# Kernel tuning notes

Measured on AMD Instinct MI355X. Metric: run time of the kernel, lower is better.

## Reference

```python
import jax, jax.numpy as jnp
import numpy as np

D = 512       # d_model
H = 8         # n_heads
L = 6         # n_blocks
DFF = 2048    # d_ffn
IN_DIM = 4096
OUT_DIM = 1000
B = 8
S = 512
DK = D // H
EPS = 1e-5
NEG = -1e9    # masked_fill value from source (-1000000000.0)

# sinusoidal positional encoding table (matches Positional_Encoding)
_pos = np.arange(5000)[:, None].astype(np.float64)
_div = np.exp(np.arange(0, D, 2) * (-np.log(10000.0) / D))
_pe = np.zeros((5000, D), np.float32)
_pe[:, 0::2] = np.sin(_pos * _div)
_pe[:, 1::2] = np.cos(_pos * _div)
PE = jnp.asarray(_pe)


def _ln(x, g, b):
    m = jnp.mean(x, -1, keepdims=True)
    v = jnp.var(x, -1, keepdims=True)
    return (x - m) * jax.lax.rsqrt(v + EPS) * g + b


def _attn(q, k, v, causal):
    # q:[B,Sq,D], k/v:[B,Sk,D] -> multi-head attention with source's quirky mask
    b, sq, _ = q.shape
    sk = k.shape[1]
    q = q.reshape(b, sq, H, DK).transpose(0, 2, 1, 3)
    k = k.reshape(b, sk, H, DK).transpose(0, 2, 1, 3)
    v = v.reshape(b, sk, H, DK).transpose(0, 2, 1, 3)
    s = jnp.einsum('bhqd,bhkd->bhqk', q, k) / jnp.sqrt(jnp.asarray(DK, q.dtype))
    mask = s != 0.0  # faithful: source masks positions where score == padding (0)
    if causal:
        mask = mask & jnp.tril(jnp.ones((sq, sk), bool))
    s = jnp.where(mask, s, NEG)
    p = jax.nn.softmax(s, axis=-1)
    o = jnp.einsum('bhqk,bhkd->bhqd', p, v)
    return o.transpose(0, 2, 1, 3).reshape(b, sq, D)


def _ffn(x, w1, b1, w2, b2):
    return jax.nn.relu(x @ w1 + b1) @ w2 + b2


def setup_inputs() -> dict:
    key = jax.random.key(0)
    ks = iter(jax.random.split(key, 40))

    def w(shape, s=0.02):
        return jax.random.normal(next(ks), shape, jnp.float32) * s

    inp = {}
    inp['x'] = jax.random.randint(next(ks), (B, S), 0, IN_DIM)
    inp['target'] = jax.random.randint(next(ks), (B,), 0, OUT_DIM)
    inp['in_emb'] = w((IN_DIM, D), 1.0)
    inp['out_emb'] = w((OUT_DIM, D), 1.0)
    # encoder params (stacked over layers)
    inp['enc_qkv_w'] = w((L, 3, D, D))
    inp['enc_qkv_b'] = w((L, 3, D))
    inp['enc_ln1_g'] = jnp.ones((L, D), jnp.float32)
    inp['enc_ln1_b'] = jnp.zeros((L, D), jnp.float32)
    inp['enc_ffn1_w'] = w((L, D, DFF))
    inp['enc_ffn1_b'] = w((L, DFF))
    inp['enc_ffn2_w'] = w((L, DFF, D))
    inp['enc_ffn2_b'] = w((L, D))
    inp['enc_ln2_g'] = jnp.ones((L, D), jnp.float32)
    inp['enc_ln2_b'] = jnp.zeros((L, D), jnp.float32)
    # decoder params
    inp['dec_qkv1_w'] = w((L, 3, D, D))
    inp['dec_qkv1_b'] = w((L, 3, D))
    inp['dec_ln1_g'] = jnp.ones((L, D), jnp.float32)
    inp['dec_ln1_b'] = jnp.zeros((L, D), jnp.float32)
    inp['dec_qkv2_w'] = w((L, 3, D, D))
    inp['dec_qkv2_b'] = w((L, 3, D))
    inp['dec_ln2_g'] = jnp.ones((L, D), jnp.float32)
    inp['dec_ln2_b'] = jnp.zeros((L, D), jnp.float32)
    inp['dec_ffn1_w'] = w((L, D, DFF))
    inp['dec_ffn1_b'] = w((L, DFF))
    inp['dec_ffn2_w'] = w((L, DFF, D))
    inp['dec_ffn2_b'] = w((L, D))
    inp['dec_ln3_g'] = jnp.ones((L, D), jnp.float32)
    inp['dec_ln3_b'] = jnp.zeros((L, D), jnp.float32)
    inp['out_w'] = w((D, OUT_DIM))
    inp['out_b'] = w((OUT_DIM,))
    return inp


def reference(x, target, in_emb, out_emb,
              enc_qkv_w, enc_qkv_b, enc_ln1_g, enc_ln1_b,
              enc_ffn1_w, enc_ffn1_b, enc_ffn2_w, enc_ffn2_b,
              enc_ln2_g, enc_ln2_b,
              dec_qkv1_w, dec_qkv1_b, dec_ln1_g, dec_ln1_b,
              dec_qkv2_w, dec_qkv2_b, dec_ln2_g, dec_ln2_b,
              dec_ffn1_w, dec_ffn1_b, dec_ffn2_w, dec_ffn2_b,
              dec_ln3_g, dec_ln3_b, out_w, out_b):
    scale = jnp.sqrt(jnp.float32(D))
    # encoder: embed tokens + positional encoding (dropout is identity at eval)
    e = in_emb[x] * scale + PE[None, :S]
    for i in range(L):
        q = e @ enc_qkv_w[i, 0] + enc_qkv_b[i, 0]
        k = e @ enc_qkv_w[i, 1] + enc_qkv_b[i, 1]
        v = e @ enc_qkv_w[i, 2] + enc_qkv_b[i, 2]
        e = _ln(_attn(q, k, v, False) + e, enc_ln1_g[i], enc_ln1_b[i])
        e = _ln(e + _ffn(e, enc_ffn1_w[i], enc_ffn1_b[i], enc_ffn2_w[i], enc_ffn2_b[i]),
                enc_ln2_g[i], enc_ln2_b[i])
    # decoder: target.unsqueeze(1) -> seq len 1
    d = out_emb[target][:, None, :] * scale + PE[None, :1]
    for i in range(L):
        q = d @ dec_qkv1_w[i, 0] + dec_qkv1_b[i, 0]
        k = d @ dec_qkv1_w[i, 1] + dec_qkv1_b[i, 1]
        v = d @ dec_qkv1_w[i, 2] + dec_qkv1_b[i, 2]
        d = _ln(_attn(q, k, v, True) + d, dec_ln1_g[i], dec_ln1_b[i])
        q = d @ dec_qkv2_w[i, 0] + dec_qkv2_b[i, 0]
        k = e @ dec_qkv2_w[i, 1] + dec_qkv2_b[i, 1]
        v = e @ dec_qkv2_w[i, 2] + dec_qkv2_b[i, 2]
        d = _ln(_attn(q, k, v, False) + d, dec_ln2_g[i], dec_ln2_b[i])
        d = _ln(d + _ffn(d, dec_ffn1_w[i], dec_ffn1_b[i], dec_ffn2_w[i], dec_ffn2_b[i]),
                dec_ln3_g[i], dec_ln3_b[i])
    return d @ out_w + out_b  # [B, 1, OUT_DIM] logits (source never applies its softmax)
```

## Files before the change

kernel.cpp:

```cpp
#include <hip/hip_runtime.h>
#include <hip/hip_bf16.h>

#define DM 512
#define NH 8
#define DK 64
#define SEQ 512
#define NB 8
#define NL 6
#define DFF 2048
#define OUTD 1000
#define EMB_SCALE 22.627416997969522f
#define PE_C (-0.017988946039015984)

typedef __bf16 bf16x8 __attribute__((ext_vector_type(8)));
typedef __bf16 bf16x4 __attribute__((ext_vector_type(4)));
typedef float f32x4 __attribute__((ext_vector_type(4)));

__device__ __forceinline__ void load16_lds(const __bf16* g, __bf16* l) {
  __builtin_amdgcn_global_load_lds(
      (const __attribute__((address_space(1))) void*)g,
      (__attribute__((address_space(3))) void*)l, 16, 0, 0);
}

__global__ __launch_bounds__(256) void pe_kernel(float* __restrict__ pe) {
  int s = blockIdx.x;
  int d2 = threadIdx.x;
  double div = exp((double)(2 * d2) * PE_C);
  double arg = (double)s * div;
  pe[(size_t)s * DM + 2 * d2] = (float)sin(arg);
  pe[(size_t)s * DM + 2 * d2 + 1] = (float)cos(arg);
}

__global__ __launch_bounds__(256) void embed_enc(const int* __restrict__ x,
                                                 const float* __restrict__ emb,
                                                 const float* __restrict__ pe,
                                                 float* __restrict__ e,
                                                 __bf16* __restrict__ eb) {
  int idx = blockIdx.x * 256 + threadIdx.x;
  int d = idx & (DM - 1);
  int bs = idx >> 9;
  int s = bs & (SEQ - 1);
  int tok = x[bs];
  float v = emb[(size_t)tok * DM + d] * EMB_SCALE + pe[(size_t)s * DM + d];
  e[idx] = v;
  eb[idx] = (__bf16)v;
}

__global__ __launch_bounds__(256) void embed_dec(const int* __restrict__ t,
                                                 const float* __restrict__ emb,
                                                 float* __restrict__ dd) {
  int idx = blockIdx.x * 256 + threadIdx.x;
  int d = idx & (DM - 1);
  int b = idx >> 9;
  float pe = (d & 1) ? 1.0f : 0.0f;
  dd[idx] = emb[(size_t)t[b] * DM + d] * EMB_SCALE + pe;
}

__global__ __launch_bounds__(256) void transpose_w(const float* __restrict__ W,
                                                   __bf16* __restrict__ WT,
                                                   int K, int N) {
  __shared__ float t[32][33];
  size_t off = (size_t)blockIdx.z * K * N;
  W += off; WT += off;
  int k0 = blockIdx.y * 32, n0 = blockIdx.x * 32;
  int tx = threadIdx.x & 7, ty = threadIdx.x >> 3;
  float4 v = *(const float4*)&W[(size_t)(k0 + ty) * N + n0 + tx * 4];
  t[ty][tx * 4 + 0] = v.x; t[ty][tx * 4 + 1] = v.y;
  t[ty][tx * 4 + 2] = v.z; t[ty][tx * 4 + 3] = v.w;
  __syncthreads();
  bf16x4 o;
  o[0] = (__bf16)t[tx * 4 + 0][ty];
  o[1] = (__bf16)t[tx * 4 + 1][ty];
  o[2] = (__bf16)t[tx * 4 + 2][ty];
  o[3] = (__bf16)t[tx * 4 + 3][ty];
  *(bf16x4*)&WT[(size_t)(n0 + ty) * K + k0 + tx * 4] = o;
}

template <int BN, bool RELU, bool WF32, bool WBF16, bool TRV>
__global__ __launch_bounds__(256) void mfma_gemm(
    const __bf16* __restrict__ A, const __bf16* __restrict__ BT,
    const float* __restrict__ bias, float* __restrict__ C,
    __bf16* __restrict__ Cb, __bf16* __restrict__ Vt, int M, int N, int K,
    long btStride, long bStride, long cStride) {
  int z = blockIdx.z;
  BT += (size_t)z * btStride;
  bias += (size_t)z * bStride;
  if (WF32) C += (size_t)z * cStride;
  if (WBF16) Cb += (size_t)z * cStride;

  constexpr int NI = BN / 32;
  __shared__ __bf16 As[128 * 64];
  __shared__ __bf16 Bs[BN * 64];

  int tid = threadIdx.x;
  int wave = tid >> 6, lane = tid & 63;
  int wm = wave >> 1, wn = wave & 1;
  int quad = lane >> 4, l16 = lane & 15;
  int rlane = lane >> 3, c8 = lane & 7;
  int m0 = blockIdx.y * 128, n0 = blockIdx.x * BN;
  int gcol = ((c8 ^ rlane) * 8);

  f32x4 acc[4][NI];
#pragma unroll
  for (int i = 0; i < 4; ++i)
#pragma unroll
    for (int j = 0; j < NI; ++j) acc[i][j] = (f32x4){0.f, 0.f, 0.f, 0.f};

  for (int k0 = 0; k0 < K; k0 += 64) {
    __syncthreads();
#pragma unroll
    for (int j = 0; j < 4; ++j) {
      int row = j * 32 + wave * 8 + rlane;
      load16_lds(&A[(size_t)(m0 + row) * K + k0 + gcol],
                 &As[(j * 32 + wave * 8) * 64]);
    }
#pragma unroll
    for (int j = 0; j < BN / 32; ++j) {
      int row = j * 32 + wave * 8 + rlane;
      load16_lds(&BT[(size_t)(n0 + row) * K + k0 + gcol],
                 &Bs[(j * 32 + wave * 8) * 64]);
    }
    __syncthreads();
#pragma unroll
    for (int kk = 0; kk < 64; kk += 32) {
      bf16x8 af[4], bf[NI];
#pragma unroll
      for (int i = 0; i < 4; ++i) {
        int row = wm * 64 + i * 16 + l16;
        af[i] = *(const bf16x8*)&As[row * 64 + ((((kk >> 3) + quad) ^ (row & 7)) * 8)];
      }
#pragma unroll
      for (int i = 0; i < NI; ++i) {
        int row = wn * (BN / 2) + i * 16 + l16;
        bf[i] = *(const bf16x8*)&Bs[row * 64 + ((((kk >> 3) + quad) ^ (row & 7)) * 8)];
      }
#pragma unroll
      for (int mi = 0; mi < 4; ++mi)
#pragma unroll
        for (int ni = 0; ni < NI; ++ni)
          acc[mi][ni] = __builtin_amdgcn_mfma_f32_16x16x32_bf16(
              af[mi], bf[ni], acc[mi][ni], 0, 0, 0);
    }
  }

#pragma unroll
  for (int ni = 0; ni < NI; ++ni) {
    int col = n0 + wn * (BN / 2) + ni * 16 + l16;
    float bv = bias[col];
    if (TRV && z == 2) {
      int b = m0 >> 9;
#pragma unroll
      for (int mi = 0; mi < 4; ++mi) {
        int srow = (m0 & 511) + wm * 64 + mi * 16 + quad * 4;
        bf16x4 pk;
#pragma unroll
        for (int r = 0; r < 4; ++r) pk[r] = (__bf16)(acc[mi][ni][r] + bv);
        *(bf16x4*)&Vt[((size_t)(b * 512 + col)) * 512 + srow] = pk;
      }
    } else {
#pragma unroll
      for (int mi = 0; mi < 4; ++mi) {
#pragma unroll
        for (int r = 0; r < 4; ++r) {
          int row = m0 + wm * 64 + mi * 16 + quad * 4 + r;
          float v = acc[mi][ni][r] + bv;
          if (RELU) v = fmaxf(v, 0.f);
          if (WF32) C[(size_t)row * N + col] = v;
          if (WBF16) Cb[(size_t)row * N + col] = (__bf16)v;
        }
      }
    }
  }
}

#define SCP 520
__global__ __launch_bounds__(256) void attn_mfma(const __bf16* __restrict__ QKV,
                                                 const __bf16* __restrict__ Vt,
                                                 float* __restrict__ O) {
  __shared__ __bf16 Sc[16 * SCP];
  __shared__ __bf16 Tt[64 * 64];

  const long ACTL = (long)NB * SEQ * DM;
  int tid = threadIdx.x;
  int wave = tid >> 6, lane = tid & 63;
  int quad = lane >> 4, l16 = lane & 15;
  int rlane = lane >> 3, c8 = lane & 7;
  int q0 = blockIdx.x * 16;
  int bh = blockIdx.y, b = bh >> 3, h = bh & 7;
  const __bf16* Q = QKV;
  const __bf16* Kp = QKV + ACTL;
  size_t baseQ = ((size_t)b * SEQ + q0) * DM + h * DK;
  size_t baseK = ((size_t)b * SEQ) * DM + h * DK;
  const __bf16* VtB = Vt + ((size_t)(b * 512 + h * 64)) * 512;
  int gcol = (c8 ^ rlane) * 8;

  bf16x8 af0 = *(const bf16x8*)&Q[baseQ + (size_t)l16 * DM + quad * 8];
  bf16x8 af1 = *(const bf16x8*)&Q[baseQ + (size_t)l16 * DM + 32 + quad * 8];

  for (int kt = 0; kt < 8; ++kt) {
    __syncthreads();
#pragma unroll
    for (int j = 0; j < 2; ++j) {
      int row = j * 32 + wave * 8 + rlane;
      load16_lds(&Kp[baseK + (size_t)(kt * 64 + row) * DM + gcol],
                 &Tt[(j * 32 + wave * 8) * 64]);
    }
    __syncthreads();
    f32x4 acc = (f32x4){0.f, 0.f, 0.f, 0.f};
    int krow = wave * 16 + l16, sw = krow & 7;
    bf16x8 b0 = *(const bf16x8*)&Tt[krow * 64 + ((quad ^ sw) * 8)];
    bf16x8 b1 = *(const bf16x8*)&Tt[krow * 64 + (((4 + quad) ^ sw) * 8)];
    acc = __builtin_amdgcn_mfma_f32_16x16x32_bf16(af0, b0, acc, 0, 0, 0);
    acc = __builtin_amdgcn_mfma_f32_16x16x32_bf16(af1, b1, acc, 0, 0, 0);
#pragma unroll
    for (int r = 0; r < 4; ++r)
      Sc[(quad * 4 + r) * SCP + kt * 64 + wave * 16 + l16] =
          (__bf16)(acc[r] * 0.125f);
  }
  __syncthreads();

#pragma unroll
  for (int rr = 0; rr < 4; ++rr) {
    int r = wave * 4 + rr;
    float v[8];
    float mx = -1e30f;
#pragma unroll
    for (int j = 0; j < 8; ++j) {
      v[j] = (float)Sc[r * SCP + j * 64 + lane];
      mx = fmaxf(mx, v[j]);
    }
    for (int o = 32; o > 0; o >>= 1) mx = fmaxf(mx, __shfl_xor(mx, o));
    float sum = 0.f;
#pragma unroll
    for (int j = 0; j < 8; ++j) { v[j] = __expf(v[j] - mx); sum += v[j]; }
    for (int o = 32; o > 0; o >>= 1) sum += __shfl_xor(sum, o);
    float inv = 1.f / sum;
#pragma unroll
    for (int j = 0; j < 8; ++j)
      Sc[r * SCP + j * 64 + lane] = (__bf16)(v[j] * inv);
  }

  f32x4 oacc = (f32x4){0.f, 0.f, 0.f, 0.f};
  for (int kt = 0; kt < 8; ++kt) {
    __syncthreads();
#pragma unroll
    for (int j = 0; j < 2; ++j) {
      int row = j * 32 + wave * 8 + rlane;
      load16_lds(&VtB[(size_t)row * 512 + kt * 64 + gcol],
                 &Tt[(j * 32 + wave * 8) * 64]);
    }
    __syncthreads();
    int drow = wave * 16 + l16, sw = drow & 7;
#pragma unroll
    for (int kk = 0; kk < 64; kk += 32) {
      bf16x8 pa = *(const bf16x8*)&Sc[l16 * SCP + kt * 64 + kk + quad * 8];
      bf16x8 vb = *(const bf16x8*)&Tt[drow * 64 + ((((kk >> 3) + quad) ^ sw) * 8)];
      oacc = __builtin_amdgcn_mfma_f32_16x16x32_bf16(pa, vb, oacc, 0, 0, 0);
    }
  }
#pragma unroll
  for (int r = 0; r < 4; ++r)
    O[((size_t)b * SEQ + q0 + quad * 4 + r) * DM + h * DK + wave * 16 + l16] =
        oacc[r];
}

template <bool RELUA>
__global__ __launch_bounds__(256) void skinny_splitk(
    const float* __restrict__ A, const float* __restrict__ abias,
    const float* __restrict__ W, float* __restrict__ C,
    int N, int K, int Kc) {
  __shared__ float As[8 * 64];
  __shared__ float red[4][8][64];

  int tid = threadIdx.x;
  int kbase = blockIdx.y * Kc;
  for (int i = tid; i < 8 * Kc; i += 256) {
    int r = i / Kc, k = i - r * Kc;
    float v = A[(size_t)r * K + kbase + k];
    if (RELUA) v = fmaxf(v + abias[kbase + k], 0.f);
    As[r * 64 + k] = v;
  }
  __syncthreads();

  int tn = tid & 63, tk = tid >> 6;
  int n = blockIdx.x * 64 + tn;
  float acc[8] = {};
  if (n < N) {
    for (int k = tk; k < Kc; k += 4) {
      float w = W[(size_t)(kbase + k) * N + n];
#pragma unroll
      for (int r = 0; r < 8; ++r) acc[r] += As[r * 64 + k] * w;
    }
  }
#pragma unroll
  for (int r = 0; r < 8; ++r) red[tk][r][tn] = acc[r];
  __syncthreads();
  if (n < N) {
#pragma unroll
    for (int rr = 0; rr < 2; ++rr) {
      int r = tk * 2 + rr;
      float s = red[0][r][tn] + red[1][r][tn] + red[2][r][tn] + red[3][r][tn];
      atomicAdd(&C[(size_t)r * N + n], s);
    }
  }
}

__global__ __launch_bounds__(256) void init_out(float* __restrict__ out,
                                                const float* __restrict__ b) {
  int i = blockIdx.x * 256 + threadIdx.x;
  if (i < NB * OUTD) out[i] = b[i % OUTD];
}

__global__ __launch_bounds__(256) void dec_cross_partial(
    const float* __restrict__ Q, const float* __restrict__ qb,
    const float* __restrict__ K, const float* __restrict__ V,
    float* __restrict__ pm, float* __restrict__ pl, float* __restrict__ po) {
  __shared__ float qs[64];
  __shared__ float red[4][64];
  __shared__ float pr[64];
  __shared__ float msh, lsh;
  int tid = threadIdx.x;
  int ks = blockIdx.x, bh = blockIdx.y;
  int b = bh >> 3, h = bh & 7;
  size_t baseQ = (size_t)b * DM + h * DK;
  size_t baseKV = ((size_t)b * SEQ + ks * 64) * DM + h * DK;

  if (tid < 64) qs[tid] = Q[baseQ + tid] + qb[h * DK + tid];
  __syncthreads();

  int key = tid & 63, sub = tid >> 6;
  const float* kp = &K[baseKV + (size_t)key * DM + sub * 16];
  float acc = 0.f;
#pragma unroll
  for (int j = 0; j < 16; ++j) acc += qs[sub * 16 + j] * kp[j];
  red[sub][key] = acc;
  __syncthreads();

  if (tid < 64) {
    float s = (red[0][tid] + red[1][tid] + red[2][tid] + red[3][tid]) * 0.125f;
    float m = s;
    for (int o = 32; o > 0; o >>= 1) m = fmaxf(m, __shfl_xor(m, o));
    float p = __expf(s - m);
    float l = p;
    for (int o = 32; o > 0; o >>= 1) l += __shfl_xor(l, o);
    pr[tid] = p;
    if (tid == 0) { msh = m; lsh = l; }
  }
  __syncthreads();

  int d = tid & 63;
  const float* vp = &V[baseKV + (size_t)(sub * 16) * DM + d];
  float oa = 0.f;
#pragma unroll
  for (int j = 0; j < 16; ++j) oa += pr[sub * 16 + j] * vp[(size_t)j * DM];
  red[sub][d] = oa;
  __syncthreads();

  if (tid < 64) {
    po[((size_t)bh * 8 + ks) * 64 + tid] =
        red[0][tid] + red[1][tid] + red[2][tid] + red[3][tid];
    if (tid == 0) { pm[bh * 8 + ks] = msh; pl[bh * 8 + ks] = lsh; }
  }
}

__global__ __launch_bounds__(64) void dec_cross_combine(
    const float* __restrict__ pm, const float* __restrict__ pl,
    const float* __restrict__ po, float* __restrict__ O) {
  int bh = blockIdx.x;
  int d = threadIdx.x;
  int b = bh >> 3, h = bh & 7;
  float M = -1e30f;
#pragma unroll
  for (int i = 0; i < 8; ++i) M = fmaxf(M, pm[bh * 8 + i]);
  float L = 0.f, o = 0.f;
#pragma unroll
  for (int i = 0; i < 8; ++i) {
    float w = __expf(pm[bh * 8 + i] - M);
    L += w * pl[bh * 8 + i];
    o += w * po[((size_t)bh * 8 + i) * 64 + d];
  }
  O[(size_t)b * DM + h * DK + d] = o / L;
}

template <bool WB>
__global__ __launch_bounds__(256) void add_ln(
    const float* __restrict__ x, const float* __restrict__ res,
    const float* __restrict__ cbias,
    const float* __restrict__ g, const float* __restrict__ beta,
    float* __restrict__ y, __bf16* __restrict__ yb) {
  int row = blockIdx.x;
  int tid = threadIdx.x;
  const float* xr = x + (size_t)row * DM;
  const float* rr = res + (size_t)row * DM;
  float b0 = cbias ? cbias[tid] : 0.f;
  float b1 = cbias ? cbias[tid + 256] : 0.f;
  float v0 = xr[tid] + b0 + rr[tid];
  float v1 = xr[tid + 256] + b1 + rr[tid + 256];
  float s = v0 + v1, sq = v0 * v0 + v1 * v1;
  for (int o = 32; o > 0; o >>= 1) {
    s += __shfl_xor(s, o);
    sq += __shfl_xor(sq, o);
  }
  __shared__ float ps[4], pq[4];
  int wv = tid >> 6;
  if ((tid & 63) == 0) { ps[wv] = s; pq[wv] = sq; }
  __syncthreads();
  s = ps[0] + ps[1] + ps[2] + ps[3];
  sq = pq[0] + pq[1] + pq[2] + pq[3];
  float mean = s * (1.f / DM);
  float var = sq * (1.f / DM) - mean * mean;
  float rstd = rsqrtf(var + 1e-5f);
  float o0 = (v0 - mean) * rstd * g[tid] + beta[tid];
  float o1 = (v1 - mean) * rstd * g[tid + 256] + beta[tid + 256];
  y[(size_t)row * DM + tid] = o0;
  y[(size_t)row * DM + tid + 256] = o1;
  if (WB) {
    yb[(size_t)row * DM + tid] = (__bf16)o0;
    yb[(size_t)row * DM + tid + 256] = (__bf16)o1;
  }
}

extern "C" void kernel_launch(void* const* d_in, const int* in_sizes, int n_in,
                              void* d_out, int out_size, void* d_ws, size_t ws_size,
                              hipStream_t stream) {
  const int* x = (const int*)d_in[0];
  const int* target = (const int*)d_in[1];
  const float* in_emb = (const float*)d_in[2];
  const float* out_emb = (const float*)d_in[3];
  const float* enc_qkv_w = (const float*)d_in[4];
  const float* enc_qkv_b = (const float*)d_in[5];
  const float* enc_ln1_g = (const float*)d_in[6];
  const float* enc_ln1_b = (const float*)d_in[7];
  const float* enc_ffn1_w = (const float*)d_in[8];
  const float* enc_ffn1_b = (const float*)d_in[9];
  const float* enc_ffn2_w = (const float*)d_in[10];
  const float* enc_ffn2_b = (const float*)d_in[11];
  const float* enc_ln2_g = (const float*)d_in[12];
  const float* enc_ln2_b = (const float*)d_in[13];
  const float* dec_qkv1_w = (const float*)d_in[14];
  const float* dec_qkv1_b = (const float*)d_in[15];
  const float* dec_ln1_g = (const float*)d_in[16];
  const float* dec_ln1_b = (const float*)d_in[17];
  const float* dec_qkv2_w = (const float*)d_in[18];
  const float* dec_qkv2_b = (const float*)d_in[19];
  const float* dec_ln2_g = (const float*)d_in[20];
  const float* dec_ln2_b = (const float*)d_in[21];
  const float* dec_ffn1_w = (const float*)d_in[22];
  const float* dec_ffn1_b = (const float*)d_in[23];
  const float* dec_ffn2_w = (const float*)d_in[24];
  const float* dec_ffn2_b = (const float*)d_in[25];
  const float* dec_ln3_g = (const float*)d_in[26];
  const float* dec_ln3_b = (const float*)d_in[27];
  const float* out_w = (const float*)d_in[28];
  const float* out_b = (const float*)d_in[29];

  const long ACTL = (long)NB * SEQ * DM;
  const int M = NB * SEQ;

  char* p = (char*)d_ws;
  float* e = (float*)p;            p += ACTL * 4;
  float* tb = (float*)p;           p += ACTL * 4;
  float* kvf = (float*)p;          p += 2 * ACTL * 4;
  float* pe = (float*)p;           p += (long)SEQ * DM * 4;
  float* dd = (float*)p;           p += NB * DM * 4;
  float* dqv = (float*)p;          p += NB * DM * 4;
  float* dqq = (float*)p;          p += NB * DM * 4;
  float* dh = (float*)p;           p += NB * DFF * 4;
  float* df = (float*)p;           p += NB * DM * 4;
  float* da = (float*)p;           p += NB * DM * 4;
  float* pm = (float*)p;           p += 64 * 8 * 4;
  float* pl = (float*)p;           p += 64 * 8 * 4;
  float* po = (float*)p;           p += 64 * 8 * 64 * 4;
  p = (char*)(((uintptr_t)p + 255) & ~(uintptr_t)255);
  __bf16* eb = (__bf16*)p;         p += ACTL * 2;
  __bf16* qkvb = (__bf16*)p;       p += 3 * ACTL * 2;
  __bf16* hbb = (__bf16*)p;        p += (long)M * DFF * 2;
  __bf16* wtq = (__bf16*)p;        p += 18L * DM * DM * 2;
  __bf16* wtf1 = (__bf16*)p;       p += 6L * DM * DFF * 2;
  __bf16* wtf2 = (__bf16*)p;       p += 6L * DFF * DM * 2;
  __bf16* wtd = (__bf16*)p;        p += 18L * DM * DM * 2;

  __bf16* vtb = qkvb + 2 * ACTL;

  const long WQS = (long)DM * DM;
  const long WFS = (long)DM * DFF;
  const size_t DEC_ZERO_BYTES = (size_t)NB * (DM + DM + DFF + DM) * 4;

  pe_kernel<<<SEQ, 256, 0, stream>>>(pe);
  transpose_w<<<dim3(16, 16, 18), 256, 0, stream>>>(enc_qkv_w, wtq, DM, DM);
  transpose_w<<<dim3(64, 16, 6), 256, 0, stream>>>(enc_ffn1_w, wtf1, DM, DFF);
  transpose_w<<<dim3(16, 64, 6), 256, 0, stream>>>(enc_ffn2_w, wtf2, DFF, DM);
  transpose_w<<<dim3(16, 16, 18), 256, 0, stream>>>(dec_qkv2_w, wtd, DM, DM);

  embed_enc<<<(M * DM) / 256, 256, 0, stream>>>(x, in_emb, pe, e, eb);
  for (int i = 0; i < NL; ++i) {
    mfma_gemm<128, false, false, true, true><<<dim3(4, 32, 3), 256, 0, stream>>>(
        eb, wtq + (size_t)i * 3 * WQS, enc_qkv_b + (size_t)i * 3 * DM,
        nullptr, qkvb, vtb, M, DM, DM, WQS, DM, ACTL);
    attn_mfma<<<dim3(SEQ / 16, NB * NH), 256, 0, stream>>>(qkvb, vtb, tb);
    add_ln<true><<<M, 256, 0, stream>>>(tb, e, nullptr, enc_ln1_g + i * DM,
                                        enc_ln1_b + i * DM, e, eb);
    mfma_gemm<128, true, false, true, false><<<dim3(16, 32, 1), 256, 0, stream>>>(
        eb, wtf1 + (size_t)i * WFS, enc_ffn1_b + (size_t)i * DFF,
        nullptr, hbb, nullptr, M, DFF, DM, 0, 0, 0);
    mfma_gemm<64, false, true, false, false><<<dim3(8, 32, 1), 256, 0, stream>>>(
        hbb, wtf2 + (size_t)i * WFS, enc_ffn2_b + (size_t)i * DM,
        tb, nullptr, nullptr, M, DM, DFF, 0, 0, 0);
    add_ln<true><<<M, 256, 0, stream>>>(tb, e, nullptr, enc_ln2_g + i * DM,
                                        enc_ln2_b + i * DM, e, eb);
  }

  embed_dec<<<(NB * DM) / 256, 256, 0, stream>>>(target, out_emb, dd);
  for (int i = 0; i < NL; ++i) {
    hipMemsetAsync(dqv, 0, DEC_ZERO_BYTES, stream);
    skinny_splitk<false><<<dim3(8, 32), 256, 0, stream>>>(
        dd, nullptr, dec_qkv1_w + ((size_t)i * 3 + 2) * WQS, dqv, DM, DM, 16);
    add_ln<false><<<NB, 256, 0, stream>>>(
        dqv, dd, dec_qkv1_b + ((size_t)i * 3 + 2) * DM,
        dec_ln1_g + i * DM, dec_ln1_b + i * DM, dd, nullptr);
    skinny_splitk<false><<<dim3(8, 32), 256, 0, stream>>>(
        dd, nullptr, dec_qkv2_w + ((size_t)i * 3 + 0) * WQS, dqq, DM, DM, 16);
    mfma_gemm<128, false, true, false, false><<<dim3(4, 32, 2), 256, 0, stream>>>(
        eb, wtd + ((size_t)i * 3 + 1) * WQS, dec_qkv2_b + ((size_t)i * 3 + 1) * DM,
        kvf, nullptr, nullptr, M, DM, DM, WQS, DM, ACTL);
    dec_cross_partial<<<dim3(8, 64), 256, 0, stream>>>(
        dqq, dec_qkv2_b + ((size_t)i * 3 + 0) * DM, kvf, kvf + ACTL, pm, pl, po);
    dec_cross_combine<<<64, 64, 0, stream>>>(pm, pl, po, da);
    add_ln<false><<<NB, 256, 0, stream>>>(
        da, dd, nullptr, dec_ln2_g + i * DM, dec_ln2_b + i * DM, dd, nullptr);
    skinny_splitk<false><<<dim3(32, 8), 256, 0, stream>>>(
        dd, nullptr, dec_ffn1_w + (size_t)i * WFS, dh, DFF, DM, 64);
    skinny_splitk<true><<<dim3(8, 32), 256, 0, stream>>>(
        dh, dec_ffn1_b + (size_t)i * DFF, dec_ffn2_w + (size_t)i * WFS,
        df, DM, DFF, 64);
    add_ln<false><<<NB, 256, 0, stream>>>(
        df, dd, dec_ffn2_b + (size_t)i * DM,
        dec_ln3_g + i * DM, dec_ln3_b + i * DM, dd, nullptr);
  }

  init_out<<<(NB * OUTD + 255) / 256, 256, 0, stream>>>((float*)d_out, out_b);
  skinny_splitk<false><<<dim3(16, 16), 256, 0, stream>>>(
      dd, nullptr, out_w, (float*)d_out, OUTD, DM, 32);
}
```

Baseline: 1.234 ms.

## Rewrite decoder path with fused bf16 GEMV kernels and batched cross-attn KV projection

All 12 decoder cross-attention K/V projections are hoisted out of the decoder loop into one batched MFMA GEMM that writes bf16 output, since they depend only on the final encoder output. The per-layer decoder work is replaced by fused kernels: a V-projection with residual add and layernorm, a query projection combined with full single-query attention, and wave-per-column bf16 GEMVs for the FFN and output layers. These drop the memset, the split-K atomics and several launches per layer. In exchange the decoder weights are transposed to bf16 up front, adding transpose work and a large extra workspace, and K/V are held in bf16, which lowers precision.

New measurement: 1.234 ms. Within noise of the previous version (-0.0%).

```diff
diff --git a/kernel.cpp b/kernel.cpp
--- a/kernel.cpp
+++ b/kernel.cpp
@@ -20,6 +20,13 @@
   __builtin_amdgcn_global_load_lds(
       (const __attribute__((address_space(1))) void*)g,
       (__attribute__((address_space(3))) void*)l, 16, 0, 0);
+}
+
+__device__ __forceinline__ float dot8(bf16x8 w, const float* a) {
+  float s = 0.f;
+#pragma unroll
+  for (int j = 0; j < 8; ++j) s += (float)w[j] * a[j];
+  return s;
 }
 
 __global__ __launch_bounds__(256) void pe_kernel(float* __restrict__ pe) {
@@ -76,15 +83,38 @@
   *(bf16x4*)&WT[(size_t)(n0 + ty) * K + k0 + tx * 4] = o;
 }
 
-template <int BN, bool RELU, bool WF32, bool WBF16, bool TRV>
+__global__ __launch_bounds__(256) void transpose_ow(const float* __restrict__ W,
+                                                    __bf16* __restrict__ WT) {
+  __shared__ float t[32][33];
+  int n0 = blockIdx.x * 32, k0 = blockIdx.y * 32;
+  int tid = threadIdx.x;
+  for (int i = tid; i < 1024; i += 256) {
+    int kk = i >> 5, nn = i & 31;
+    t[kk][nn] = (n0 + nn < OUTD) ? W[(size_t)(k0 + kk) * OUTD + n0 + nn] : 0.f;
+  }
+  __syncthreads();
+  for (int i = tid; i < 1024; i += 256) {
+    int nn = i >> 5, kk = i & 31;
+    if (n0 + nn < OUTD)
+      WT[(size_t)(n0 + nn) * DM + k0 + kk] = (__bf16)t[kk][nn];
+  }
+}
+
+template <int BN, bool RELU, bool WF32, bool WBF16, bool TRV, bool KVM>
 __global__ __launch_bounds__(256) void mfma_gemm(
     const __bf16* __restrict__ A, const __bf16* __restrict__ BT,
     const float* __restrict__ bias, float* __restrict__ C,
     __bf16* __restrict__ Cb, __bf16* __restrict__ Vt, int M, int N, int K,
     long btStride, long bStride, long cStride) {
   int z = blockIdx.z;
-  BT += (size_t)z * btStride;
-  bias += (size_t)z * bStride;
+  if (KVM) {
+    long idx = (long)(z >> 1) * 3 + 1 + (z & 1);
+    BT += idx * btStride;
+    bias += idx * bStride;
+  } else {
+    BT += (size_t)z * btStride;
+    bias += (size_t)z * bStride;
+  }
   if (WF32) C += (size_t)z * cStride;
   if (WBF16) Cb += (size_t)z * cStride;
 
@@ -262,124 +292,6 @@
   for (int r = 0; r < 4; ++r)
     O[((size_t)b * SEQ + q0 + quad * 4 + r) * DM + h * DK + wave * 16 + l16] =
         oacc[r];
-}
-
-template <bool RELUA>
-__global__ __launch_bounds__(256) void skinny_splitk(
-    const float* __restrict__ A, const float* __restrict__ abias,
-    const float* __restrict__ W, float* __restrict__ C,
-    int N, int K, int Kc) {
-  __shared__ float As[8 * 64];
-  __shared__ float red[4][8][64];
-
-  int tid = threadIdx.x;
-  int kbase = blockIdx.y * Kc;
-  for (int i = tid; i < 8 * Kc; i += 256) {
-    int r = i / Kc, k = i - r * Kc;
-    float v = A[(size_t)r * K + kbase + k];
-    if (RELUA) v = fmaxf(v + abias[kbase + k], 0.f);
-    As[r * 64 + k] = v;
-  }
-  __syncthreads();
-
-  int tn = tid & 63, tk = tid >> 6;
-  int n = blockIdx.x * 64 + tn;
-  float acc[8] = {};
-  if (n < N) {
-    for (int k = tk; k < Kc; k += 4) {
-      float w = W[(size_t)(kbase + k) * N + n];
-#pragma unroll
-      for (int r = 0; r < 8; ++r) acc[r] += As[r * 64 + k] * w;
-    }
-  }
-#pragma unroll
-  for (int r = 0; r < 8; ++r) red[tk][r][tn] = acc[r];
-  __syncthreads();
-  if (n < N) {
-#pragma unroll
-    for (int rr = 0; rr < 2; ++rr) {
-      int r = tk * 2 + rr;
-      float s = red[0][r][tn] + red[1][r][tn] + red[2][r][tn] + red[3][r][tn];
-      atomicAdd(&C[(size_t)r * N + n], s);
-    }
-  }
-}
-
-__global__ __launch_bounds__(256) void init_out(float* __restrict__ out,
-                                                const float* __restrict__ b) {
-  int i = blockIdx.x * 256 + threadIdx.x;
-  if (i < NB * OUTD) out[i] = b[i % OUTD];
-}
-
-__global__ __launch_bounds__(256) void dec_cross_partial(
-    const float* __restrict__ Q, const float* __restrict__ qb,
-    const float* __restrict__ K, const float* __restrict__ V,
-    float* __restrict__ pm, float* __restrict__ pl, float* __restrict__ po) {
-  __shared__ float qs[64];
-  __shared__ float red[4][64];
-  __shared__ float pr[64];
-  __shared__ float msh, lsh;
-  int tid = threadIdx.x;
-  int ks = blockIdx.x, bh = blockIdx.y;
-  int b = bh >> 3, h = bh & 7;
-  size_t baseQ = (size_t)b * DM + h * DK;
-  size_t baseKV = ((size_t)b * SEQ + ks * 64) * DM + h * DK;
-
-  if (tid < 64) qs[tid] = Q[baseQ + tid] + qb[h * DK + tid];
-  __syncthreads();
-
-  int key = tid & 63, sub = tid >> 6;
-  const float* kp = &K[baseKV + (size_t)key * DM + sub * 16];
-  float acc = 0.f;
-#pragma unroll
-  for (int j = 0; j < 16; ++j) acc += qs[sub * 16 + j] * kp[j];
-  red[sub][key] = acc;
-  __syncthreads();
-
-  if (tid < 64) {
-    float s = (red[0][tid] + red[1][tid] + red[2][tid] + red[3][tid]) * 0.125f;
-    float m = s;
-    for (int o = 32; o > 0; o >>= 1) m = fmaxf(m, __shfl_xor(m, o));
-    float p = __expf(s - m);
-    float l = p;
-    for (int o = 32; o > 0; o >>= 1) l += __shfl_xor(l, o);
-    pr[tid] = p;
-    if (tid == 0) { msh = m; lsh = l; }
-  }
-  __syncthreads();
-
-  int d = tid & 63;
-  const float* vp = &V[baseKV + (size_t)(sub * 16) * DM + d];
-  float oa = 0.f;
-#pragma unroll
-  for (int j = 0; j < 16; ++j) oa += pr[sub * 16 + j] * vp[(size_t)j * DM];
-  red[sub][d] = oa;
-  __syncthreads();
-
-  if (tid < 64) {
-    po[((size_t)bh * 8 + ks) * 64 + tid] =
-        red[0][tid] + red[1][tid] + red[2][tid] + red[3][tid];
-    if (tid == 0) { pm[bh * 8 + ks] = msh; pl[bh * 8 + ks] = lsh; }
-  }
-}
-
-__global__ __launch_bounds__(64) void dec_cross_combine(
-    const float* __restrict__ pm, const float* __restrict__ pl,
-    const float* __restrict__ po, float* __restrict__ O) {
-  int bh = blockIdx.x;
-  int d = threadIdx.x;
-  int b = bh >> 3, h = bh & 7;
-  float M = -1e30f;
-#pragma unroll
-  for (int i = 0; i < 8; ++i) M = fmaxf(M, pm[bh * 8 + i]);
-  float L = 0.f, o = 0.f;
-#pragma unroll
-  for (int i = 0; i < 8; ++i) {
-    float w = __expf(pm[bh * 8 + i] - M);
-    L += w * pl[bh * 8 + i];
-    o += w * po[((size_t)bh * 8 + i) * 64 + d];
-  }
-  O[(size_t)b * DM + h * DK + d] = o / L;
 }
 
 template <bool WB>
@@ -417,6 +329,190 @@
   if (WB) {
     yb[(size_t)row * DM + tid] = (__bf16)o0;
     yb[(size_t)row * DM + tid + 256] = (__bf16)o1;
+  }
+}
+
+
+__global__ __launch_bounds__(256) void dec_vln(
+    float* __restrict__ dd, const __bf16* __restrict__ WvT,
+    const float* __restrict__ bv, const float* __restrict__ g,
+    const float* __restrict__ beta) {
+  __shared__ float arow[DM];
+  int r = blockIdx.x, tid = threadIdx.x;
+  arow[tid] = dd[(size_t)r * DM + tid];
+  arow[tid + 256] = dd[(size_t)r * DM + tid + 256];
+  __syncthreads();
+  float out[2];
+#pragma unroll
+  for (int cc = 0; cc < 2; ++cc) {
+    int c = tid + cc * 256;
+    const __bf16* w = &WvT[(size_t)c * DM];
+    float acc = 0.f;
+#pragma unroll 4
+    for (int k = 0; k < DM; k += 8) acc += dot8(*(const bf16x8*)&w[k], &arow[k]);
+    out[cc] = arow[c] + acc + bv[c];
+  }
+  float s = out[0] + out[1], sq = out[0] * out[0] + out[1] * out[1];
+  for (int o = 32; o > 0; o >>= 1) { s += __shfl_xor(s, o); sq += __shfl_xor(sq, o); }
+  __shared__ float ps[4], pq[4];
+  int wv = tid >> 6;
+  if ((tid & 63) == 0) { ps[wv] = s; pq[wv] = sq; }
+  __syncthreads();
+  s = ps[0] + ps[1] + ps[2] + ps[3];
+  sq = pq[0] + pq[1] + pq[2] + pq[3];
+  float mean = s * (1.f / DM);
+  float rstd = rsqrtf(sq * (1.f / DM) - mean * mean + 1e-5f);
+  dd[(size_t)r * DM + tid] = (out[0] - mean) * rstd * g[tid] + beta[tid];
+  dd[(size_t)r * DM + tid + 256] = (out[1] - mean) * rstd * g[tid + 256] + beta[tid + 256];
+}
+
+__global__ __launch_bounds__(256) void dec_qattn(
+    const float* __restrict__ dd, const __bf16* __restrict__ WqT,
+    const float* __restrict__ qb, const __bf16* __restrict__ Kb,
+    const __bf16* __restrict__ Vb, float* __restrict__ da) {
+  __shared__ float arow[DM];
+  __shared__ float red[4][64];
+  __shared__ float q[64];
+  __shared__ float sc[SEQ];
+  __shared__ float wred[4];
+  __shared__ float smax, ssum;
+
+  int bh = blockIdx.x, b = bh >> 3, h = bh & 7;
+  int tid = threadIdx.x, lane = tid & 63, wave = tid >> 6;
+  arow[tid] = dd[(size_t)b * DM + tid];
+  arow[tid + 256] = dd[(size_t)b * DM + tid + 256];
+  __syncthreads();
+
+  {
+    int c = tid & 63, s = tid >> 6;
+    const __bf16* w = &WqT[(size_t)(h * 64 + c) * DM + s * 128];
+    float acc = 0.f;
+#pragma unroll
+    for (int k = 0; k < 128; k += 8) acc += dot8(*(const bf16x8*)&w[k], &arow[s * 128 + k]);
+    red[s][c] = acc;
+  }
+  __syncthreads();
+  if (tid < 64) q[tid] = red[0][tid] + red[1][tid] + red[2][tid] + red[3][tid] + qb[h * 64 + tid];
+  __syncthreads();
+
+  for (int key = tid; key < SEQ; key += 256) {
+    const __bf16* kp = &Kb[((size_t)b * SEQ + key) * DM + h * 64];
+    float acc = 0.f;
+#pragma unroll
+    for (int k = 0; k < 64; k += 8) acc += dot8(*(const bf16x8*)&kp[k], &q[k]);
+    sc[key] = acc * 0.125f;
+  }
+  __syncthreads();
+  float m = -1e30f;
+  for (int j = tid; j < SEQ; j += 256) m = fmaxf(m, sc[j]);
+  for (int o = 32; o > 0; o >>= 1) m = fmaxf(m, __shfl_xor(m, o));
+  if (lane == 0) wred[wave] = m;
+  __syncthreads();
+  m = fmaxf(fmaxf(wred[0], wred[1]), fmaxf(wred[2], wred[3]));
+  float sum = 0.f;
+  for (int j = tid; j < SEQ; j += 256) {
+    float p = __expf(sc[j] - m);
+    sc[j] = p;
+    sum += p;
+  }
+  for (int o = 32; o > 0; o >>= 1) sum += __shfl_xor(sum, o);
+  __syncthreads();
+  if (lane == 0) wred[wave] = sum;
+  __syncthreads();
+  float inv = 1.f / (wred[0] + wred[1] + wred[2] + wred[3]);
+
+  {
+    int d = tid & 63, s = tid >> 6;
+    float acc = 0.f;
+    const __bf16* vp = &Vb[((size_t)b * SEQ + s * 128) * DM + h * 64 + d];
+#pragma unroll 8
+    for (int k = 0; k < 128; ++k) acc += sc[s * 128 + k] * (float)vp[(size_t)k * DM];
+    red[s][d] = acc;
+  }
+  __syncthreads();
+  if (tid < 64)
+    da[(size_t)b * DM + h * 64 + tid] =
+        (red[0][tid] + red[1][tid] + red[2][tid] + red[3][tid]) * inv;
+}
+
+__global__ __launch_bounds__(256) void dec_ffn1(
+    const float* __restrict__ dd, const __bf16* __restrict__ W1T,
+    const float* __restrict__ b1, float* __restrict__ h) {
+  __shared__ float a[8][DM];
+  int tid = threadIdx.x, lane = tid & 63, wave = tid >> 6;
+  for (int i = tid; i < 8 * DM; i += 256) a[i >> 9][i & 511] = dd[i];
+  __syncthreads();
+  int col = blockIdx.x * 4 + wave;
+  bf16x8 w = *(const bf16x8*)&W1T[(size_t)col * DM + lane * 8];
+  float acc[8];
+#pragma unroll
+  for (int r = 0; r < 8; ++r) acc[r] = dot8(w, &a[r][lane * 8]);
+#pragma unroll
+  for (int r = 0; r < 8; ++r)
+    for (int o = 32; o > 0; o >>= 1) acc[r] += __shfl_xor(acc[r], o);
+  if (lane == 0) {
+    float bb = b1[col];
+#pragma unroll
+    for (int r = 0; r < 8; ++r) h[(size_t)r * DFF + col] = fmaxf(acc[r] + bb, 0.f);
+  }
+}
+
+__global__ __launch_bounds__(256) void dec_ffn2(
+    const float* __restrict__ h, const __bf16* __restrict__ W2T,
+    const float* __restrict__ b2, float* __restrict__ df) {
+  __shared__ float red[4][8];
+  int tid = threadIdx.x, lane = tid & 63, wave = tid >> 6;
+  int c = wave >> 1, half = wave & 1;
+  int col = blockIdx.x * 2 + c;
+  int k0 = half * 1024 + lane * 8;
+  bf16x8 w0 = *(const bf16x8*)&W2T[(size_t)col * DFF + k0];
+  bf16x8 w1 = *(const bf16x8*)&W2T[(size_t)col * DFF + k0 + 512];
+  float acc[8];
+#pragma unroll
+  for (int r = 0; r < 8; ++r) {
+    float4 h0a = *(const float4*)&h[(size_t)r * DFF + k0];
+    float4 h0b = *(const float4*)&h[(size_t)r * DFF + k0 + 4];
+    float4 h1a = *(const float4*)&h[(size_t)r * DFF + k0 + 512];
+    float4 h1b = *(const float4*)&h[(size_t)r * DFF + k0 + 516];
+    float hh0[8] = {h0a.x, h0a.y, h0a.z, h0a.w, h0b.x, h0b.y, h0b.z, h0b.w};
+    float hh1[8] = {h1a.x, h1a.y, h1a.z, h1a.w, h1b.x, h1b.y, h1b.z, h1b.w};
+    acc[r] = dot8(w0, hh0) + dot8(w1, hh1);
+  }
+#pragma unroll
+  for (int r = 0; r < 8; ++r)
+    for (int o = 32; o > 0; o >>= 1) acc[r] += __shfl_xor(acc[r], o);
+  if (lane == 0) {
+#pragma unroll
+    for (int r = 0; r < 8; ++r) red[wave][r] = acc[r];
+  }
+  __syncthreads();
+  if (tid < 16) {
+    int cc = tid >> 3, r = tid & 7;
+    int ocol = blockIdx.x * 2 + cc;
+    df[(size_t)r * DM + ocol] =
+        red[cc * 2][r] + red[cc * 2 + 1][r] + b2[ocol];
+  }
+}
+
+__global__ __launch_bounds__(256) void dec_out(
+    const float* __restrict__ dd, const __bf16* __restrict__ WoT,
+    const float* __restrict__ ob, float* __restrict__ out) {
+  __shared__ float a[8][DM];
+  int tid = threadIdx.x, lane = tid & 63, wave = tid >> 6;
+  for (int i = tid; i < 8 * DM; i += 256) a[i >> 9][i & 511] = dd[i];
+  __syncthreads();
+  int col = blockIdx.x * 4 + wave;
+  bf16x8 w = *(const bf16x8*)&WoT[(size_t)col * DM + lane * 8];
+  float acc[8];
+#pragma unroll
+  for (int r = 0; r < 8; ++r) acc[r] = dot8(w, &a[r][lane * 8]);
+#pragma unroll
+  for (int r = 0; r < 8; ++r)
+    for (int o = 32; o > 0; o >>= 1) acc[r] += __shfl_xor(acc[r], o);
+  if (lane == 0) {
+    float bb = ob[col];
+#pragma unroll
+    for (int r = 0; r < 8; ++r) out[(size_t)r * OUTD + col] = acc[r] + bb;
   }
 }
 
@@ -456,89 +552,81 @@
 
   const long ACTL = (long)NB * SEQ * DM;
   const int M = NB * SEQ;
+  const long WQS = (long)DM * DM;
+  const long WFS = (long)DM * DFF;
 
   char* p = (char*)d_ws;
   float* e = (float*)p;            p += ACTL * 4;
   float* tb = (float*)p;           p += ACTL * 4;
-  float* kvf = (float*)p;          p += 2 * ACTL * 4;
   float* pe = (float*)p;           p += (long)SEQ * DM * 4;
   float* dd = (float*)p;           p += NB * DM * 4;
-  float* dqv = (float*)p;          p += NB * DM * 4;
-  float* dqq = (float*)p;          p += NB * DM * 4;
+  float* da = (float*)p;           p += NB * DM * 4;
   float* dh = (float*)p;           p += NB * DFF * 4;
   float* df = (float*)p;           p += NB * DM * 4;
-  float* da = (float*)p;           p += NB * DM * 4;
-  float* pm = (float*)p;           p += 64 * 8 * 4;
-  float* pl = (float*)p;           p += 64 * 8 * 4;
-  float* po = (float*)p;           p += 64 * 8 * 64 * 4;
   p = (char*)(((uintptr_t)p + 255) & ~(uintptr_t)255);
   __bf16* eb = (__bf16*)p;         p += ACTL * 2;
   __bf16* qkvb = (__bf16*)p;       p += 3 * ACTL * 2;
   __bf16* hbb = (__bf16*)p;        p += (long)M * DFF * 2;
-  __bf16* wtq = (__bf16*)p;        p += 18L * DM * DM * 2;
-  __bf16* wtf1 = (__bf16*)p;       p += 6L * DM * DFF * 2;
-  __bf16* wtf2 = (__bf16*)p;       p += 6L * DFF * DM * 2;
-  __bf16* wtd = (__bf16*)p;        p += 18L * DM * DM * 2;
+  __bf16* kvb = (__bf16*)p;        p += 12L * ACTL * 2;
+  __bf16* wtq = (__bf16*)p;        p += 18L * WQS * 2;
+  __bf16* wtf1 = (__bf16*)p;       p += 6L * WFS * 2;
+  __bf16* wtf2 = (__bf16*)p;       p += 6L * WFS * 2;
+  __bf16* wtd = (__bf16*)p;        p += 18L * WQS * 2;
+  __bf16* wtd1 = (__bf16*)p;       p += 18L * WQS * 2;
+  __bf16* wf1t = (__bf16*)p;       p += 6L * WFS * 2;
+  __bf16* wf2t = (__bf16*)p;       p += 6L * WFS * 2;
+  __bf16* wot = (__bf16*)p;        p += (long)OUTD * DM * 2;
 
   __bf16* vtb = qkvb + 2 * ACTL;
-
-  const long WQS = (long)DM * DM;
-  const long WFS = (long)DM * DFF;
-  const size_t DEC_ZERO_BYTES = (size_t)NB * (DM + DM + DFF + DM) * 4;
 
   pe_kernel<<<SEQ, 256, 0, stream>>>(pe);
   transpose_w<<<dim3(16, 16, 18), 256, 0, stream>>>(enc_qkv_w, wtq, DM, DM);
   transpose_w<<<dim3(64, 16, 6), 256, 0, stream>>>(enc_ffn1_w, wtf1, DM, DFF);
   transpose_w<<<dim3(16, 64, 6), 256, 0, stream>>>(enc_ffn2_w, wtf2, DFF, DM);
   transpose_w<<<dim3(16, 16, 18), 256, 0, stream>>>(dec_qkv2_w, wtd, DM, DM);
+  transpose_w<<<dim3(16, 16, 18), 256, 0, stream>>>(dec_qkv1_w, wtd1, DM, DM);
+  transpose_w<<<dim3(64, 16, 6), 256, 0, stream>>>(dec_ffn1_w, wf1t, DM, DFF);
+  transpose_w<<<dim3(16, 64, 6), 256, 0, stream>>>(dec_ffn2_w, wf2t, DFF, DM);
+  transpose_ow<<<dim3(32, 16), 256, 0, stream>>>(out_w, wot);
 
   embed_enc<<<(M * DM) / 256, 256, 0, stream>>>(x, in_emb, pe, e, eb);
   for (int i = 0; i < NL; ++i) {
-    mfma_gemm<128, false, false, true, true><<<dim3(4, 32, 3), 256, 0, stream>>>(
+    mfma_gemm<128, false, false, true, true, false><<<dim3(4, 32, 3), 256, 0, stream>>>(
         eb, wtq + (size_t)i * 3 * WQS, enc_qkv_b + (size_t)i * 3 * DM,
         nullptr, qkvb, vtb, M, DM, DM, WQS, DM, ACTL);
     attn_mfma<<<dim3(SEQ / 16, NB * NH), 256, 0, stream>>>(qkvb, vtb, tb);
     add_ln<true><<<M, 256, 0, stream>>>(tb, e, nullptr, enc_ln1_g + i * DM,
                                         enc_ln1_b + i * DM, e, eb);
-    mfma_gemm<128, true, false, true, false><<<dim3(16, 32, 1), 256, 0, stream>>>(
+    mfma_gemm<128, true, false, true, false, false><<<dim3(16, 32, 1), 256, 0, stream>>>(
         eb, wtf1 + (size_t)i * WFS, enc_ffn1_b + (size_t)i * DFF,
         nullptr, hbb, nullptr, M, DFF, DM, 0, 0, 0);
-    mfma_gemm<64, false, true, false, false><<<dim3(8, 32, 1), 256, 0, stream>>>(
+    mfma_gemm<64, false, true, false, false, false><<<dim3(8, 32, 1), 256, 0, stream>>>(
         hbb, wtf2 + (size_t)i * WFS, enc_ffn2_b + (size_t)i * DM,
         tb, nullptr, nullptr, M, DM, DFF, 0, 0, 0);
     add_ln<true><<<M, 256, 0, stream>>>(tb, e, nullptr, enc_ln2_g + i * DM,
                                         enc_ln2_b + i * DM, e, eb);
   }
 
+  mfma_gemm<128, false, false, true, false, true><<<dim3(4, 32, 12), 256, 0, stream>>>(
+      eb, wtd, dec_qkv2_b, nullptr, kvb, nullptr, M, DM, DM, WQS, DM, ACTL);
+
   embed_dec<<<(NB * DM) / 256, 256, 0, stream>>>(target, out_emb, dd);
   for (int i = 0; i < NL; ++i) {
-    hipMemsetAsync(dqv, 0, DEC_ZERO_BYTES, stream);
-    skinny_splitk<false><<<dim3(8, 32), 256, 0, stream>>>(
-        dd, nullptr, dec_qkv1_w + ((size_t)i * 3 + 2) * WQS, dqv, DM, DM, 16);
-    add_ln<false><<<NB, 256, 0, stream>>>(
-        dqv, dd, dec_qkv1_b + ((size_t)i * 3 + 2) * DM,
-        dec_ln1_g + i * DM, dec_ln1_b + i * DM, dd, nullptr);
-    skinny_splitk<false><<<dim3(8, 32), 256, 0, stream>>>(
-        dd, nullptr, dec_qkv2_w + ((size_t)i * 3 + 0) * WQS, dqq, DM, DM, 16);
-    mfma_gemm<128, false, true, false, false><<<dim3(4, 32, 2), 256, 0, stream>>>(
-        eb, wtd + ((size_t)i * 3 + 1) * WQS, dec_qkv2_b + ((size_t)i * 3 + 1) * DM,
-        kvf, nullptr, nullptr, M, DM, DM, WQS, DM, ACTL);
-    dec_cross_partial<<<dim3(8, 64), 256, 0, stream>>>(
-        dqq, dec_qkv2_b + ((size_t)i * 3 + 0) * DM, kvf, kvf + ACTL, pm, pl, po);
-    dec_cross_combine<<<64, 64, 0, stream>>>(pm, pl, po, da);
+    dec_vln<<<8, 256, 0, stream>>>(
+        dd, wtd1 + ((size_t)i * 3 + 2) * WQS, dec_qkv1_b + ((size_t)i * 3 + 2) * DM,
+        dec_ln1_g + i * DM, dec_ln1_b + i * DM);
+    dec_qattn<<<64, 256, 0, stream>>>(
+        dd, wtd + (size_t)i * 3 * WQS, dec_qkv2_b + (size_t)i * 3 * DM,
+        kvb + (size_t)i * 2 * ACTL, kvb + ((size_t)i * 2 + 1) * ACTL, da);
     add_ln<false><<<NB, 256, 0, stream>>>(
         da, dd, nullptr, dec_ln2_g + i * DM, dec_ln2_b + i * DM, dd, nullptr);
-    skinny_splitk<false><<<dim3(32, 8), 256, 0, stream>>>(
-        dd, nullptr, dec_ffn1_w + (size_t)i * WFS, dh, DFF, DM, 64);
-    skinny_splitk<true><<<dim3(8, 32), 256, 0, stream>>>(
-        dh, dec_ffn1_b + (size_t)i * DFF, dec_ffn2_w + (size_t)i * WFS,
-        df, DM, DFF, 64);
+    dec_ffn1<<<DFF / 4, 256, 0, stream>>>(
+        dd, wf1t + (size_t)i * WFS, dec_ffn1_b + (size_t)i * DFF, dh);
+    dec_ffn2<<<DM / 2, 256, 0, stream>>>(
+        dh, wf2t + (size_t)i * WFS, dec_ffn2_b + (size_t)i * DM, df);
     add_ln<false><<<NB, 256, 0, stream>>>(
-        df, dd, dec_ffn2_b + (size_t)i * DM,
-        dec_ln3_g + i * DM, dec_ln3_b + i * DM, dd, nullptr);
-  }
-
-  init_out<<<(NB * OUTD + 255) / 256, 256, 0, stream>>>((float*)d_out, out_b);
-  skinny_splitk<false><<<dim3(16, 16), 256, 0, stream>>>(
-      dd, nullptr, out_w, (float*)d_out, OUTD, DM, 32);
-}
+        df, dd, nullptr, dec_ln3_g + i * DM, dec_ln3_b + i * DM, dd, nullptr);
+  }
+
+  dec_out<<<OUTD / 4, 256, 0, stream>>>(dd, wot, out_b, (float*)d_out);
+}
```
